# Performance work log

Measured on AMD Instinct MI355X. Metric: run time of the kernel, lower is better.

## Reference

```python
import jax, jax.numpy as jnp
import numpy as np
import itertools

B, H, W = 64, 256, 256
K = 8

def _make_consts():
    dct = np.zeros((8, 8, 8, 8), np.float32)
    idct = np.zeros((8, 8, 8, 8), np.float32)
    for x, y, u, v in itertools.product(range(8), repeat=4):
        dct[x, y, u, v] = np.cos((2 * x + 1) * u * np.pi / 16) * np.cos((2 * y + 1) * v * np.pi / 16)
        idct[x, y, u, v] = np.cos((2 * u + 1) * x * np.pi / 16) * np.cos((2 * v + 1) * y * np.pi / 16)
    alpha = np.array([1.0 / np.sqrt(2)] + [1.0] * 7, np.float32)
    aa = np.outer(alpha, alpha).astype(np.float32)
    y_table = np.array([[16, 11, 10, 16, 24, 40, 51, 61], [12, 12, 14, 19, 26, 58, 60, 55], [14, 13, 16, 24, 40, 57, 69, 56], [14, 17, 22, 29, 51, 87, 80, 62], [18, 22, 37, 56, 68, 109, 103, 77], [24, 35, 55, 64, 81, 104, 113, 92], [49, 64, 78, 87, 103, 121, 120, 101], [72, 92, 95, 98, 112, 100, 103, 99]], np.float32).T
    c_table = np.full((8, 8), 99.0, np.float32)
    c_table[:4, :4] = np.array([[17, 18, 24, 47], [18, 21, 26, 66], [24, 26, 56, 99], [47, 66, 99, 99]], np.float32).T
    rgb2ycc = np.array([[0.299, 0.587, 0.114], [-0.168736, -0.331264, 0.5], [0.5, -0.418688, -0.081312]], np.float32).T
    ycc2rgb = np.array([[1.0, 0.0, 1.402], [1.0, -0.344136, -0.714136], [1.0, 1.772, 0.0]], np.float32).T
    return tuple(map(jnp.asarray, (dct, idct, aa, y_table, c_table, rgb2ycc, ycc2rgb)))

DCT_T, IDCT_T, AA, Y_TABLE, C_TABLE, RGB2YCC, YCC2RGB = _make_consts()

def _to_patches(x):
    # [B,h,w] -> [B, (h//8)*(w//8), 8, 8]
    b, h, w = x.shape
    return x.reshape(b, h // K, K, w // K, K).transpose(0, 1, 3, 2, 4).reshape(b, -1, K, K)

def _from_patches(p, h, w):
    # [B, n, 8, 8] -> [B, h, w]
    b = p.shape[0]
    return p.reshape(b, h // K, w // K, K, K).transpose(0, 1, 3, 2, 4).reshape(b, h, w)

def _channel(comp, table, rv, lam):
    # comp: [B,h,w]. DCT -> quantize with noisy rounding -> dequantize -> IDCT. Returns patches [B,n,8,8].
    p = _to_patches(comp) - 128.0
    f = 0.25 * AA * jnp.einsum('bnxy,xyuv->bnuv', p, DCT_T)          # forward DCT-II per 8x8 block
    q = f / table
    # noisy_round(x, noise) = x + lam*(noise - 0.5), noise = 0.5 + 0.5*rv  =>  x + lam*0.5*rv
    q = q + lam[:, None, None, None] * (0.5 * rv)
    d = q * table
    return 0.25 * jnp.einsum('bnxy,xyuv->bnuv', d * AA, IDCT_T) + 128.0

def _jpeg(pixel_inp, rv_y, rv_cb, rv_cr, epsilon):
    img = jnp.transpose(pixel_inp, (0, 3, 2, 1))  # torch.transpose(image, 1, 3) -> [B,W,H,3]
    h, w = img.shape[1], img.shape[2]
    ycc = jnp.einsum('bhwc,cd->bhwd', img, RGB2YCC) + jnp.array([0.0, 128.0, 128.0], jnp.float32)
    y = ycc[..., 0]
    cb = ycc[..., 1].reshape(-1, h // 2, 2, w // 2, 2).mean(axis=(2, 4))  # 4:2:0 avg_pool2d(k=2)
    cr = ycc[..., 2].reshape(-1, h // 2, 2, w // 2, 2).mean(axis=(2, 4))
    y = _from_patches(_channel(y, Y_TABLE, rv_y, epsilon), h, w)
    cb = _from_patches(_channel(cb, C_TABLE, rv_cb, epsilon), h // 2, w // 2)
    cr = _from_patches(_channel(cr, C_TABLE, rv_cr, epsilon), h // 2, w // 2)
    cb = jnp.repeat(jnp.repeat(cb, 2, axis=1), 2, axis=2)
    cr = jnp.repeat(jnp.repeat(cr, 2, axis=1), 2, axis=2)
    out = jnp.stack((y, cb, cr), axis=-1)
    rgb = jnp.einsum('bhwc,cd->bhwd', out + jnp.array([0.0, -128.0, -128.0], jnp.float32), YCC2RGB)
    rgb = jnp.clip(rgb, 0.0, 255.0)
    return jnp.transpose(rgb, (0, 3, 2, 1))

def setup_inputs() -> dict:
    key = jax.random.key(0)
    k1, k2, k3, k4, k5 = jax.random.split(key, 5)
    pixel_inp = jax.random.uniform(k1, (B, 3, H, W), jnp.float32) * 255.0
    rv_y = jax.random.uniform(k2, (B, (H // 8) * (W // 8), 8, 8), jnp.float32) * 2.0 - 1.0
    rv_cb = jax.random.uniform(k3, (B, (H // 16) * (W // 16), 8, 8), jnp.float32) * 2.0 - 1.0
    rv_cr = jax.random.uniform(k4, (B, (H // 16) * (W // 16), 8, 8), jnp.float32) * 2.0 - 1.0
    epsilon = jax.random.uniform(k5, (B,), jnp.float32) * 8.0
    return {'pixel_inp': pixel_inp, 'rv_y': rv_y, 'rv_cb': rv_cb, 'rv_cr': rv_cr, 'epsilon': epsilon}

def reference(pixel_inp, rv_y, rv_cb, rv_cr, epsilon):
    return _jpeg(pixel_inp, rv_y, rv_cb, rv_cr, epsilon)
```

## Files before the change

kernel.cpp:

```cpp
#include <hip/hip_runtime.h>


__constant__ float YBT[64] = {
  16,12,14,14,18,24,49,72,
  11,12,13,17,22,35,64,92,
  10,14,16,22,37,55,78,95,
  16,19,24,29,56,64,87,98,
  24,26,40,51,68,81,103,112,
  40,58,57,87,109,104,121,100,
  51,60,69,80,103,113,120,103,
  61,55,56,62,77,92,101,99};

__constant__ float CBTc[64] = {
  17,18,24,47,99,99,99,99,
  18,21,26,66,99,99,99,99,
  24,26,56,99,99,99,99,99,
  47,66,99,99,99,99,99,99,
  99,99,99,99,99,99,99,99,
  99,99,99,99,99,99,99,99,
  99,99,99,99,99,99,99,99,
  99,99,99,99,99,99,99,99};

__device__ __forceinline__ void idct8(const float* __restrict__ t,
                                      float* __restrict__ o) {
    const float r  = 0.70710678118654752f;
    const float a  = 0.92387953251128674f;
    const float bq = 0.38268343236508977f;
    const float c1 = 0.98078528040323044f;
    const float c3 = 0.83146961230254524f;
    const float c5 = 0.55557023301960222f;
    const float c7 = 0.19509032201612827f;
    const float p  = fmaf(r,  t[4], t[0]);
    const float m  = fmaf(-r, t[4], t[0]);
    const float q  = fmaf(a,  t[2],  bq*t[6]);
    const float s  = fmaf(bq, t[2],  -a*t[6]);
    const float E0 = p + q, E3 = p - q, E1 = m + s, E2 = m - s;
    const float O0 = fmaf(c1,t[1], fmaf( c3,t[3], fmaf( c5,t[5],  c7*t[7])));
    const float O1 = fmaf(c3,t[1], fmaf(-c7,t[3], fmaf(-c1,t[5], -c5*t[7])));
    const float O2 = fmaf(c5,t[1], fmaf(-c1,t[3], fmaf( c7,t[5],  c3*t[7])));
    const float O3 = fmaf(c7,t[1], fmaf(-c5,t[3], fmaf( c3,t[5], -c1*t[7])));
    o[0]=E0+O0; o[7]=E0-O0; o[1]=E1+O1; o[6]=E1-O1;
    o[2]=E2+O2; o[5]=E2-O2; o[3]=E3+O3; o[4]=E3-O3;
}

__global__ __launch_bounds__(256) void jpeg_kernel(
    const float* __restrict__ pix,
    const float* __restrict__ rvy,
    const float* __restrict__ rvcb,
    const float* __restrict__ rvcr,
    const float* __restrict__ epsv,
    float* __restrict__ out)
{
    __shared__ float sY[32*72];
    __shared__ float sC[16*72];
    __shared__ float pool[2*576];

    const int tid = threadIdx.x;
    const int b   = blockIdx.y;
    const int ti  = blockIdx.x >> 3;
    const int tj  = blockIdx.x & 7;
    const int qi  = tid & 7;
    const int dj  = tid >> 3;

    const float eps8 = epsv[b] * 0.125f;
    const float RT   = 0.70710678118654752f;

    const int i0 = ti*64 + qi*8;
    const int j  = tj*32 + dj;
    const size_t pb = (size_t)b*196608 + (size_t)j*256 + i0;
    const float4 rA = *(const float4*)(pix + pb);
    const float4 rB = *(const float4*)(pix + pb + 4);
    const float4 gA = *(const float4*)(pix + pb + 65536);
    const float4 gB = *(const float4*)(pix + pb + 65540);
    const float4 bA = *(const float4*)(pix + pb + 131072);
    const float4 bB = *(const float4*)(pix + pb + 131076);

    float rr[8] = {rA.x,rA.y,rA.z,rA.w,rB.x,rB.y,rB.z,rB.w};
    float gg[8] = {gA.x,gA.y,gA.z,gA.w,gB.x,gB.y,gB.z,gB.w};
    float bb[8] = {bA.x,bA.y,bA.z,bA.w,bB.x,bB.y,bB.z,bB.w};
    float yv[8], cbv[8], crv[8];
    #pragma unroll
    for (int c = 0; c < 8; ++c) {
        yv[c]  = fmaf(0.299f, rr[c], fmaf(0.587f, gg[c], 0.114f*bb[c]));
        cbv[c] = fmaf(-0.168736f, rr[c], fmaf(-0.331264f, gg[c], 0.5f*bb[c]));
        crv[c] = fmaf(0.5f, rr[c], fmaf(-0.418688f, gg[c], -0.081312f*bb[c]));
    }
    float cbs[4], crs[4];
    #pragma unroll
    for (int k = 0; k < 4; ++k) {
        cbs[k] = cbv[2*k] + cbv[2*k+1];
        crs[k] = crv[2*k] + crv[2*k+1];
        cbs[k] += __shfl_xor(cbs[k], 8);
        crs[k] += __shfl_xor(crs[k], 8);
    }
    if ((dj & 1) == 0) {
        const int cj = dj >> 1;
        float* pp = &pool[cj*36 + qi*4];
        *(float4*)pp        = make_float4(0.25f*cbs[0],0.25f*cbs[1],0.25f*cbs[2],0.25f*cbs[3]);
        *(float4*)(pp+576)  = make_float4(0.25f*crs[0],0.25f*crs[1],0.25f*crs[2],0.25f*crs[3]);
    }

    {
        const int nl = tid >> 3;
        const int xc = tid & 7;
        const int bx = nl >> 2, by = nl & 3;
        const size_t ng = (size_t)((ti*8 + bx)*32 + tj*4 + by);
        const float* rp = rvy + ((size_t)b*1024 + ng)*64 + xc*8;
        const float4 v0 = *(const float4*)rp;
        const float4 v1 = *(const float4*)(rp + 4);
        const float4 y0 = *(const float4*)&YBT[xc*8];
        const float4 y1 = *(const float4*)&YBT[xc*8 + 4];
        const float aax = (xc == 0 ? RT : 1.0f) * eps8;
        float t[8];
        t[0] = v0.x * (y0.x * aax * RT);
        t[1] = v0.y * (y0.y * aax);
        t[2] = v0.z * (y0.z * aax);
        t[3] = v0.w * (y0.w * aax);
        t[4] = v1.x * (y1.x * aax);
        t[5] = v1.y * (y1.y * aax);
        t[6] = v1.z * (y1.z * aax);
        t[7] = v1.w * (y1.w * aax);
        float o[8];
        idct8(t, o);
        const int swz = (bx & 1) * 4;
        float* wY = &sY[nl*72 + (xc ^ swz)];
        #pragma unroll
        for (int v = 0; v < 8; ++v) wY[v*8] = o[v];
    }
    if (tid < 128) {
        const int nc = tid >> 3;
        const int xc = tid & 7;
        const int ch = nc >> 3, idx = nc & 7, cbx = idx >> 1, cby = idx & 1;
        const size_t ng = (size_t)((ti*4 + cbx)*16 + tj*2 + cby);
        const float* __restrict__ rvc = ch ? rvcr : rvcb;
        const float* rp = rvc + ((size_t)b*256 + ng)*64 + xc*8;
        const float4 v0 = *(const float4*)rp;
        const float4 v1 = *(const float4*)(rp + 4);
        const float4 y0 = *(const float4*)&CBTc[xc*8];
        const float4 y1 = *(const float4*)&CBTc[xc*8 + 4];
        const float aax = (xc == 0 ? RT : 1.0f) * eps8;
        float t[8];
        t[0] = v0.x * (y0.x * aax * RT);
        t[1] = v0.y * (y0.y * aax);
        t[2] = v0.z * (y0.z * aax);
        t[3] = v0.w * (y0.w * aax);
        t[4] = v1.x * (y1.x * aax);
        t[5] = v1.y * (y1.y * aax);
        t[6] = v1.z * (y1.z * aax);
        t[7] = v1.w * (y1.w * aax);
        float o[8];
        idct8(t, o);
        const int swz = ((nc >> 2) & 1) * 4;
        float* wC = &sC[nc*72 + (xc ^ swz)];
        #pragma unroll
        for (int v = 0; v < 8; ++v) wC[v*8] = o[v];
    }
    __syncthreads();

    float yn[8];
    {
        const int n2 = qi*4 + (dj >> 3);
        const int v2 = dj & 7;
        const int s2 = (qi & 1) * 4;
        const float* rY = &sY[n2*72 + v2*8];
        const float4 lo = *(const float4*)(rY + s2);
        const float4 hi = *(const float4*)(rY + (s2 ^ 4));
        float t[8] = {lo.x,lo.y,lo.z,lo.w,hi.x,hi.y,hi.z,hi.w};
        idct8(t, yn);
    }
    if (tid < 128) {
        const int nc2 = tid >> 3;
        const int vc2 = tid & 7;
        const int sc2 = ((nc2 >> 2) & 1) * 4;
        const float* rC = &sC[nc2*72 + vc2*8];
        const float4 lo = *(const float4*)(rC + sc2);
        const float4 hi = *(const float4*)(rC + (sc2 ^ 4));
        float t[8] = {lo.x,lo.y,lo.z,lo.w,hi.x,hi.y,hi.z,hi.w};
        float cn[8];
        idct8(t, cn);
        const int ch = nc2 >> 3, idx = nc2 & 7, cbx = idx >> 1, cby = idx & 1;
        const int cj = cby*8 + vc2;
        float* pp = &pool[ch*576 + cj*36 + cbx*8];
        const float4 p0 = *(const float4*)pp;
        const float4 p1 = *(const float4*)(pp + 4);
        *(float4*)pp       = make_float4(p0.x+cn[0], p0.y+cn[1], p0.z+cn[2], p0.w+cn[3]);
        *(float4*)(pp + 4) = make_float4(p1.x+cn[4], p1.y+cn[5], p1.z+cn[6], p1.w+cn[7]);
    }
    __syncthreads();

    const int cjf = dj >> 1;
    const float4 cb4 = *(const float4*)&pool[cjf*36 + qi*4];
    const float4 cr4 = *(const float4*)&pool[576 + cjf*36 + qi*4];
    const float cbf[8] = {cb4.x,cb4.x,cb4.y,cb4.y,cb4.z,cb4.z,cb4.w,cb4.w};
    const float crf[8] = {cr4.x,cr4.x,cr4.y,cr4.y,cr4.z,cr4.z,cr4.w,cr4.w};
    float ro[8], go[8], bo[8];
    #pragma unroll
    for (int c = 0; c < 8; ++c) {
        const float yf = yv[c] + yn[c];
        float r_ = fmaf(1.402f, crf[c], yf);
        float g_ = fmaf(-0.344136f, cbf[c], fmaf(-0.714136f, crf[c], yf));
        float b_ = fmaf(1.772f, cbf[c], yf);
        ro[c] = fminf(fmaxf(r_, 0.0f), 255.0f);
        go[c] = fminf(fmaxf(g_, 0.0f), 255.0f);
        bo[c] = fminf(fmaxf(b_, 0.0f), 255.0f);
    }
    *(float4*)(out + pb)          = make_float4(ro[0],ro[1],ro[2],ro[3]);
    *(float4*)(out + pb + 4)      = make_float4(ro[4],ro[5],ro[6],ro[7]);
    *(float4*)(out + pb + 65536)  = make_float4(go[0],go[1],go[2],go[3]);
    *(float4*)(out + pb + 65540)  = make_float4(go[4],go[5],go[6],go[7]);
    *(float4*)(out + pb + 131072) = make_float4(bo[0],bo[1],bo[2],bo[3]);
    *(float4*)(out + pb + 131076) = make_float4(bo[4],bo[5],bo[6],bo[7]);
}

extern "C" void kernel_launch(void* const* d_in, const int* in_sizes, int n_in,
                              void* d_out, int out_size, void* d_ws, size_t ws_size,
                              hipStream_t stream) {
    const float* pix  = (const float*)d_in[0];
    const float* rvy  = (const float*)d_in[1];
    const float* rvcb = (const float*)d_in[2];
    const float* rvcr = (const float*)d_in[3];
    const float* eps  = (const float*)d_in[4];
    const int B = in_sizes[4];
    dim3 grid(32, B);
    jpeg_kernel<<<grid, 256, 0, stream>>>(pix, rvy, rvcb, rvcr, eps, (float*)d_out);
}
```

Baseline: 26.56 us.

## Halve per-block tile to 32x32 pixels, doubling grid and reshaping LDS stages

Each block now covers a 32x32 pixel tile with four pixels per thread instead of 64x32 with eight, and the grid doubles to 64 blocks per image. The noise loads and first IDCT pass are issued before the pixel loads. The second IDCT pass writes Y results into a new LDS buffer (nylds) that the final colour-conversion stage reads back. The aim is more blocks in flight and lower register pressure to hide memory latency, at the cost of idle lanes in the IDCT stages (only 192 of 256 threads active) and an extra LDS round trip.

```diff
diff --git a/kernel.cpp b/kernel.cpp
--- a/kernel.cpp
+++ b/kernel.cpp
@@ -51,151 +51,134 @@
     const float* __restrict__ epsv,
     float* __restrict__ out)
 {
-    __shared__ float sY[32*72];
-    __shared__ float sC[16*72];
-    __shared__ float pool[2*576];
+    __shared__ float sY[16*68];
+    __shared__ float sC[8*68];
+    __shared__ float nylds[32*36];
+    __shared__ float pool[2*320];
 
     const int tid = threadIdx.x;
+    const int qi  = tid & 7;
+    const int dj  = tid >> 3;
     const int b   = blockIdx.y;
     const int ti  = blockIdx.x >> 3;
     const int tj  = blockIdx.x & 7;
-    const int qi  = tid & 7;
-    const int dj  = tid >> 3;
 
     const float eps8 = epsv[b] * 0.125f;
     const float RT   = 0.70710678118654752f;
 
-    const int i0 = ti*64 + qi*8;
+    float4 v0, v1, t0, t1;
+    int nl = 0;
+    const int xc = tid & 7;
+    const bool isY = tid < 128, isC = (tid >= 128) && (tid < 192);
+    if (isY) {
+        nl = tid >> 3;
+        const int bx = nl >> 2, by = nl & 3;
+        const int ng = (ti*4 + bx)*32 + (tj*4 + by);
+        const float* rp = rvy + ((size_t)b*1024 + ng)*64 + xc*8;
+        v0 = *(const float4*)rp;
+        v1 = *(const float4*)(rp + 4);
+        t0 = *(const float4*)&YBT[xc*8];
+        t1 = *(const float4*)&YBT[xc*8 + 4];
+    } else if (isC) {
+        nl = (tid - 128) >> 3;
+        const int ch = nl >> 2, idx = nl & 3, cbx = idx >> 1, cby = idx & 1;
+        const int ng = (ti*2 + cbx)*16 + (tj*2 + cby);
+        const float* __restrict__ rvc = ch ? rvcr : rvcb;
+        const float* rp = rvc + ((size_t)b*256 + ng)*64 + xc*8;
+        v0 = *(const float4*)rp;
+        v1 = *(const float4*)(rp + 4);
+        t0 = *(const float4*)&CBTc[xc*8];
+        t1 = *(const float4*)&CBTc[xc*8 + 4];
+    }
+
+    const int i0 = ti*32 + qi*4;
     const int j  = tj*32 + dj;
     const size_t pb = (size_t)b*196608 + (size_t)j*256 + i0;
-    const float4 rA = *(const float4*)(pix + pb);
-    const float4 rB = *(const float4*)(pix + pb + 4);
-    const float4 gA = *(const float4*)(pix + pb + 65536);
-    const float4 gB = *(const float4*)(pix + pb + 65540);
-    const float4 bA = *(const float4*)(pix + pb + 131072);
-    const float4 bB = *(const float4*)(pix + pb + 131076);
-
-    float rr[8] = {rA.x,rA.y,rA.z,rA.w,rB.x,rB.y,rB.z,rB.w};
-    float gg[8] = {gA.x,gA.y,gA.z,gA.w,gB.x,gB.y,gB.z,gB.w};
-    float bb[8] = {bA.x,bA.y,bA.z,bA.w,bB.x,bB.y,bB.z,bB.w};
-    float yv[8], cbv[8], crv[8];
+    const float4 rP = *(const float4*)(pix + pb);
+    const float4 gP = *(const float4*)(pix + pb + 65536);
+    const float4 bP = *(const float4*)(pix + pb + 131072);
+
+    if (isY || isC) {
+        const float aax = (xc == 0 ? RT : 1.0f) * eps8;
+        float t[8];
+        t[0] = v0.x * (t0.x * aax * RT);
+        t[1] = v0.y * (t0.y * aax);
+        t[2] = v0.z * (t0.z * aax);
+        t[3] = v0.w * (t0.w * aax);
+        t[4] = v1.x * (t1.x * aax);
+        t[5] = v1.y * (t1.y * aax);
+        t[6] = v1.z * (t1.z * aax);
+        t[7] = v1.w * (t1.w * aax);
+        float o[8];
+        idct8(t, o);
+        float* ws = (isY ? sY : sC) + nl*68 + xc*8;
+        *(float4*)ws       = make_float4(o[0], o[1], o[2], o[3]);
+        *(float4*)(ws + 4) = make_float4(o[4], o[5], o[6], o[7]);
+    }
+
+    const float rr[4] = {rP.x, rP.y, rP.z, rP.w};
+    const float gg[4] = {gP.x, gP.y, gP.z, gP.w};
+    const float bb[4] = {bP.x, bP.y, bP.z, bP.w};
+    float yv[4], cbv[4], crv[4];
     #pragma unroll
-    for (int c = 0; c < 8; ++c) {
+    for (int c = 0; c < 4; ++c) {
         yv[c]  = fmaf(0.299f, rr[c], fmaf(0.587f, gg[c], 0.114f*bb[c]));
         cbv[c] = fmaf(-0.168736f, rr[c], fmaf(-0.331264f, gg[c], 0.5f*bb[c]));
         crv[c] = fmaf(0.5f, rr[c], fmaf(-0.418688f, gg[c], -0.081312f*bb[c]));
     }
-    float cbs[4], crs[4];
-    #pragma unroll
-    for (int k = 0; k < 4; ++k) {
-        cbs[k] = cbv[2*k] + cbv[2*k+1];
-        crs[k] = crv[2*k] + crv[2*k+1];
-        cbs[k] += __shfl_xor(cbs[k], 8);
-        crs[k] += __shfl_xor(crs[k], 8);
-    }
+    float cb01 = cbv[0] + cbv[1], cb23 = cbv[2] + cbv[3];
+    float cr01 = crv[0] + crv[1], cr23 = crv[2] + crv[3];
+    cb01 += __shfl_xor(cb01, 8);
+    cb23 += __shfl_xor(cb23, 8);
+    cr01 += __shfl_xor(cr01, 8);
+    cr23 += __shfl_xor(cr23, 8);
     if ((dj & 1) == 0) {
-        const int cj = dj >> 1;
-        float* pp = &pool[cj*36 + qi*4];
-        *(float4*)pp        = make_float4(0.25f*cbs[0],0.25f*cbs[1],0.25f*cbs[2],0.25f*cbs[3]);
-        *(float4*)(pp+576)  = make_float4(0.25f*crs[0],0.25f*crs[1],0.25f*crs[2],0.25f*crs[3]);
-    }
-
-    {
-        const int nl = tid >> 3;
-        const int xc = tid & 7;
-        const int bx = nl >> 2, by = nl & 3;
-        const size_t ng = (size_t)((ti*8 + bx)*32 + tj*4 + by);
-        const float* rp = rvy + ((size_t)b*1024 + ng)*64 + xc*8;
-        const float4 v0 = *(const float4*)rp;
-        const float4 v1 = *(const float4*)(rp + 4);
-        const float4 y0 = *(const float4*)&YBT[xc*8];
-        const float4 y1 = *(const float4*)&YBT[xc*8 + 4];
-        const float aax = (xc == 0 ? RT : 1.0f) * eps8;
+        float* pp = &pool[(dj >> 1)*20 + qi*2];
+        *(float2*)pp         = make_float2(0.25f*cb01, 0.25f*cb23);
+        *(float2*)(pp + 320) = make_float2(0.25f*cr01, 0.25f*cr23);
+    }
+    __syncthreads();
+
+    if (tid < 128) {
+        const int n2 = tid >> 3, v2 = tid & 7;
+        const float* rs = &sY[n2*68 + v2];
         float t[8];
-        t[0] = v0.x * (y0.x * aax * RT);
-        t[1] = v0.y * (y0.y * aax);
-        t[2] = v0.z * (y0.z * aax);
-        t[3] = v0.w * (y0.w * aax);
-        t[4] = v1.x * (y1.x * aax);
-        t[5] = v1.y * (y1.y * aax);
-        t[6] = v1.z * (y1.z * aax);
-        t[7] = v1.w * (y1.w * aax);
+        #pragma unroll
+        for (int x = 0; x < 8; ++x) t[x] = rs[x*8];
         float o[8];
         idct8(t, o);
-        const int swz = (bx & 1) * 4;
-        float* wY = &sY[nl*72 + (xc ^ swz)];
+        const int jj = (n2 & 3)*8 + v2;
+        float* wn = &nylds[jj*36 + (n2 >> 2)*8];
+        *(float4*)wn       = make_float4(o[0], o[1], o[2], o[3]);
+        *(float4*)(wn + 4) = make_float4(o[4], o[5], o[6], o[7]);
+    } else if (tid < 192) {
+        const int c2 = tid - 128;
+        const int nc2 = c2 >> 3, vc2 = c2 & 7;
+        const float* rs = &sC[nc2*68 + vc2];
+        float t[8];
         #pragma unroll
-        for (int v = 0; v < 8; ++v) wY[v*8] = o[v];
-    }
-    if (tid < 128) {
-        const int nc = tid >> 3;
-        const int xc = tid & 7;
-        const int ch = nc >> 3, idx = nc & 7, cbx = idx >> 1, cby = idx & 1;
-        const size_t ng = (size_t)((ti*4 + cbx)*16 + tj*2 + cby);
-        const float* __restrict__ rvc = ch ? rvcr : rvcb;
-        const float* rp = rvc + ((size_t)b*256 + ng)*64 + xc*8;
-        const float4 v0 = *(const float4*)rp;
-        const float4 v1 = *(const float4*)(rp + 4);
-        const float4 y0 = *(const float4*)&CBTc[xc*8];
-        const float4 y1 = *(const float4*)&CBTc[xc*8 + 4];
-        const float aax = (xc == 0 ? RT : 1.0f) * eps8;
-        float t[8];
-        t[0] = v0.x * (y0.x * aax * RT);
-        t[1] = v0.y * (y0.y * aax);
-        t[2] = v0.z * (y0.z * aax);
-        t[3] = v0.w * (y0.w * aax);
-        t[4] = v1.x * (y1.x * aax);
-        t[5] = v1.y * (y1.y * aax);
-        t[6] = v1.z * (y1.z * aax);
-        t[7] = v1.w * (y1.w * aax);
+        for (int x = 0; x < 8; ++x) t[x] = rs[x*8];
         float o[8];
         idct8(t, o);
-        const int swz = ((nc >> 2) & 1) * 4;
-        float* wC = &sC[nc*72 + (xc ^ swz)];
-        #pragma unroll
-        for (int v = 0; v < 8; ++v) wC[v*8] = o[v];
-    }
-    __syncthreads();
-
-    float yn[8];
-    {
-        const int n2 = qi*4 + (dj >> 3);
-        const int v2 = dj & 7;
-        const int s2 = (qi & 1) * 4;
-        const float* rY = &sY[n2*72 + v2*8];
-        const float4 lo = *(const float4*)(rY + s2);
-        const float4 hi = *(const float4*)(rY + (s2 ^ 4));
-        float t[8] = {lo.x,lo.y,lo.z,lo.w,hi.x,hi.y,hi.z,hi.w};
-        idct8(t, yn);
-    }
-    if (tid < 128) {
-        const int nc2 = tid >> 3;
-        const int vc2 = tid & 7;
-        const int sc2 = ((nc2 >> 2) & 1) * 4;
-        const float* rC = &sC[nc2*72 + vc2*8];
-        const float4 lo = *(const float4*)(rC + sc2);
-        const float4 hi = *(const float4*)(rC + (sc2 ^ 4));
-        float t[8] = {lo.x,lo.y,lo.z,lo.w,hi.x,hi.y,hi.z,hi.w};
-        float cn[8];
-        idct8(t, cn);
-        const int ch = nc2 >> 3, idx = nc2 & 7, cbx = idx >> 1, cby = idx & 1;
-        const int cj = cby*8 + vc2;
-        float* pp = &pool[ch*576 + cj*36 + cbx*8];
+        const int ch = nc2 >> 2, idx = nc2 & 3, cbx = idx >> 1, cby = idx & 1;
+        float* pp = &pool[ch*320 + (cby*8 + vc2)*20 + cbx*8];
         const float4 p0 = *(const float4*)pp;
         const float4 p1 = *(const float4*)(pp + 4);
-        *(float4*)pp       = make_float4(p0.x+cn[0], p0.y+cn[1], p0.z+cn[2], p0.w+cn[3]);
-        *(float4*)(pp + 4) = make_float4(p1.x+cn[4], p1.y+cn[5], p1.z+cn[6], p1.w+cn[7]);
+        *(float4*)pp       = make_float4(p0.x+o[0], p0.y+o[1], p0.z+o[2], p0.w+o[3]);
+        *(float4*)(pp + 4) = make_float4(p1.x+o[4], p1.y+o[5], p1.z+o[6], p1.w+o[7]);
     }
     __syncthreads();
 
-    const int cjf = dj >> 1;
-    const float4 cb4 = *(const float4*)&pool[cjf*36 + qi*4];
-    const float4 cr4 = *(const float4*)&pool[576 + cjf*36 + qi*4];
-    const float cbf[8] = {cb4.x,cb4.x,cb4.y,cb4.y,cb4.z,cb4.z,cb4.w,cb4.w};
-    const float crf[8] = {cr4.x,cr4.x,cr4.y,cr4.y,cr4.z,cr4.z,cr4.w,cr4.w};
-    float ro[8], go[8], bo[8];
+    const float4 yn4 = *(const float4*)&nylds[dj*36 + qi*4];
+    const int cj = dj >> 1;
+    const float2 cbp = *(const float2*)&pool[cj*20 + qi*2];
+    const float2 crp = *(const float2*)&pool[320 + cj*20 + qi*2];
+    const float yn[4]  = {yn4.x, yn4.y, yn4.z, yn4.w};
+    const float cbf[4] = {cbp.x, cbp.x, cbp.y, cbp.y};
+    const float crf[4] = {crp.x, crp.x, crp.y, crp.y};
+    float ro[4], go[4], bo[4];
     #pragma unroll
-    for (int c = 0; c < 8; ++c) {
+    for (int c = 0; c < 4; ++c) {
         const float yf = yv[c] + yn[c];
         float r_ = fmaf(1.402f, crf[c], yf);
         float g_ = fmaf(-0.344136f, cbf[c], fmaf(-0.714136f, crf[c], yf));
@@ -204,12 +187,9 @@
         go[c] = fminf(fmaxf(g_, 0.0f), 255.0f);
         bo[c] = fminf(fmaxf(b_, 0.0f), 255.0f);
     }
-    *(float4*)(out + pb)          = make_float4(ro[0],ro[1],ro[2],ro[3]);
-    *(float4*)(out + pb + 4)      = make_float4(ro[4],ro[5],ro[6],ro[7]);
-    *(float4*)(out + pb + 65536)  = make_float4(go[0],go[1],go[2],go[3]);
-    *(float4*)(out + pb + 65540)  = make_float4(go[4],go[5],go[6],go[7]);
-    *(float4*)(out + pb + 131072) = make_float4(bo[0],bo[1],bo[2],bo[3]);
-    *(float4*)(out + pb + 131076) = make_float4(bo[4],bo[5],bo[6],bo[7]);
+    *(float4*)(out + pb)          = make_float4(ro[0], ro[1], ro[2], ro[3]);
+    *(float4*)(out + pb + 65536)  = make_float4(go[0], go[1], go[2], go[3]);
+    *(float4*)(out + pb + 131072) = make_float4(bo[0], bo[1], bo[2], bo[3]);
 }
 
 extern "C" void kernel_launch(void* const* d_in, const int* in_sizes, int n_in,
@@ -221,6 +201,6 @@
     const float* rvcr = (const float*)d_in[3];
     const float* eps  = (const float*)d_in[4];
     const int B = in_sizes[4];
-    dim3 grid(32, B);
+    dim3 grid(64, B);
     jpeg_kernel<<<grid, 256, 0, stream>>>(pix, rvy, rvcb, rvcr, eps, (float*)d_out);
 }
```

New measurement: 24.52 us, median of 2. -7.7%, faster.
